# Kernel tuning notes

Hardware: AMD Instinct MI355X
Metric: run time of the kernel (lower is better)

The kernel has to match this reference:

```python
import jax, jax.numpy as jnp
import numpy as np
from jax import lax

TAU = 10.0
THR = 1.0
ALPHA = float(np.exp(-1.0 / TAU))  # leak factor exp(-dt/tau), dt=1


def conv2d(x, w, pad):
    # x: [N,C,H,W], w: [O,I,kh,kw]
    return lax.conv_general_dilated(
        x, w, window_strides=(1, 1), padding=[(pad, pad), (pad, pad)],
        dimension_numbers=('NCHW', 'OIHW', 'NCHW'))


def avgpool(x, k):
    n, c, h, w = x.shape
    return x.reshape(n, c, h // k, k, w // k, k).mean(axis=(3, 5))


def exp_leak(x):
    # x: [T, ...]; v[t] = alpha*v[t-1] + x[t]; outputs membrane each step
    def step(v, xt):
        v = ALPHA * v + xt
        return v, v
    _, y = lax.scan(step, jnp.zeros_like(x[0]), x)
    return y


def lif(x):
    # LIF with SingleSpike + MembraneSubtract reset (norm_input=False)
    def step(v, xt):
        v = ALPHA * v + xt
        s = (v >= THR).astype(v.dtype)
        return v - s * THR, s
    _, s = lax.scan(step, jnp.zeros_like(x[0]), x)
    return s


def forward(x, conv1_w, conv2_w, lin_w):
    B, T = x.shape[:2]
    h = avgpool(conv2d(x.reshape(B * T, 2, 32, 32), conv1_w, 2), 4)  # [BT,4,8,8]
    h = h.reshape(B, T, 4, 8, 8).swapaxes(0, 1)                       # [T,B,4,8,8]
    h = lif(exp_leak(h)).swapaxes(0, 1).reshape(B * T, 4, 8, 8)
    h = avgpool(conv2d(h, conv2_w, 1), 2)                             # [BT,8,4,4]
    h = h.reshape(B, T, 8, 4, 4).swapaxes(0, 1)                       # [T,B,8,4,4]
    h = lif(exp_leak(h)).swapaxes(0, 1).reshape(B, T, 8 * 4 * 4)      # [B,T,128]
    return jnp.einsum('btf,of->bto', h, lin_w)                        # [B,T,2]


def setup_inputs() -> dict:
    key = jax.random.key(0)
    k1, k2, k3, k4 = jax.random.split(key, 4)
    B, T = 128, 100
    x = jax.random.uniform(k1, (B, T, 2, 32, 32), dtype=jnp.float32)
    conv1_w = jax.random.normal(k2, (4, 2, 5, 5), dtype=jnp.float32) / np.sqrt(2 * 5 * 5)
    conv2_w = jax.random.normal(k3, (8, 4, 3, 3), dtype=jnp.float32) / np.sqrt(4 * 3 * 3)
    lin_w = jax.random.normal(k4, (2, 128), dtype=jnp.float32) / np.sqrt(128)
    return {'x': x, 'conv1_w': conv1_w, 'conv2_w': conv2_w, 'lin_w': lin_w}


def reference(x, conv1_w, conv2_w, lin_w):
    return forward(x, conv1_w, conv2_w, lin_w)
```

## Files before the change

kernel.cpp:

```cpp
#include <hip/hip_runtime.h>

#define ALPHA 0.90483741803595957f

__global__ void prep_weights(const float* __restrict__ w1, const float* __restrict__ w2,
                             float* __restrict__ w1e, float* __restrict__ w2e) {
    int idx = blockIdx.x * 256 + threadIdx.x;
    if (idx < 512) {
        int v = idx & 7, u = (idx >> 3) & 7, ch = (idx >> 6) & 1, oc = idx >> 7;
        float s = 0.f;
        for (int a = 0; a < 5; ++a) {
            int i = u - a; if (i < 0 || i > 3) continue;
            for (int b = 0; b < 5; ++b) {
                int j = v - b; if (j < 0 || j > 3) continue;
                s += w1[((oc * 2 + ch) * 5 + a) * 5 + b];
            }
        }
        w1e[idx] = s * (1.f / 16.f);
    } else if (idx < 1024) {
        int k = idx - 512;
        int v = k & 3, u = (k >> 2) & 3, ch = (k >> 4) & 3, oc = k >> 6;
        float s = 0.f;
        for (int a = 0; a < 3; ++a) {
            int i = u - a; if (i < 0 || i > 1) continue;
            for (int b = 0; b < 3; ++b) {
                int j = v - b; if (j < 0 || j > 1) continue;
                s += w2[((oc * 4 + ch) * 3 + a) * 3 + b];
            }
        }
        w2e[k] = s * 0.25f;
    }
}

__global__ __launch_bounds__(256) void conv1_pool(const float* __restrict__ x,
                                                  const float* __restrict__ w1e,
                                                  float* __restrict__ y1) {
    __shared__ __align__(16) float tile[4][2][36][36];
    int tid = threadIdx.x;

    float4* t4 = (float4*)&tile[0][0][0][0];
    #pragma unroll
    for (int k = 0; k < 11; ++k) {
        int i = tid + k * 256;
        if (i < 2592) t4[i] = make_float4(0.f, 0.f, 0.f, 0.f);
    }
    __syncthreads();

    int li = tid >> 6, pos = tid & 63;
    long gi = (long)blockIdx.x * 4 + li;
    const float* src = x + gi * 2048;
    #pragma unroll
    for (int k = 0; k < 8; ++k) {
        int e = k * 256 + pos * 4;
        float4 d = *(const float4*)(src + e);
        int ch = e >> 10, rem = e & 1023, r = rem >> 5, c = rem & 31;
        float* dst = &tile[li][ch][r + 2][c + 2];
        dst[0] = d.x; dst[1] = d.y; dst[2] = d.z; dst[3] = d.w;
    }
    __syncthreads();

    int p = pos >> 3, q = pos & 7;
    float acc0 = 0.f, acc1 = 0.f, acc2 = 0.f, acc3 = 0.f;
    #pragma unroll
    for (int ch = 0; ch < 2; ++ch) {
        #pragma unroll
        for (int r = 0; r < 8; ++r) {
            const float* row = &tile[li][ch][4 * p + r][4 * q];
            float4 a = *(const float4*)row;
            float4 b = *(const float4*)(row + 4);
            float in[8] = {a.x, a.y, a.z, a.w, b.x, b.y, b.z, b.w};
            #pragma unroll
            for (int c = 0; c < 8; ++c) {
                float xi = in[c];
                acc0 += w1e[((0 * 2 + ch) * 8 + r) * 8 + c] * xi;
                acc1 += w1e[((1 * 2 + ch) * 8 + r) * 8 + c] * xi;
                acc2 += w1e[((2 * 2 + ch) * 8 + r) * 8 + c] * xi;
                acc3 += w1e[((3 * 2 + ch) * 8 + r) * 8 + c] * xi;
            }
        }
    }
    float* dst = y1 + gi * 256 + pos;
    dst[0] = acc0; dst[64] = acc1; dst[128] = acc2; dst[192] = acc3;
}

__global__ __launch_bounds__(64, 1) void fused_wave(const float* __restrict__ y1,
                                                    const float* __restrict__ w2e,
                                                    const float* __restrict__ lw,
                                                    float* __restrict__ out) {
    __shared__ float tEv[808];
    __shared__ float tOd[808];
    int lane = threadIdx.x;
    int b = blockIdx.x;

    #pragma unroll
    for (int k = 0; k < 13; ++k) {
        int i = lane + k * 64;
        if (i < 808) { tEv[i] = 0.f; tOd[i] = 0.f; }
    }

    int r1 = lane >> 3, c1 = lane & 7;
    int posq = ((r1 + 1) * 10 + (c1 + 1)) * 4;
    float* wrE0 = &tEv[posq];
    float* wrE1 = &tEv[404 + posq];
    float* wrO0 = &tOd[posq];
    float* wrO1 = &tOd[404 + posq];

    int oc = lane >> 4, p = (lane >> 2) & 3, q = lane & 3;

    float wa[64], wb[64];
    #pragma unroll
    for (int k = 0; k < 16; ++k) {
        float4 ta = *(const float4*)(w2e + oc * 64 + k * 4);
        float4 tb = *(const float4*)(w2e + (oc + 4) * 64 + k * 4);
        wa[k * 4 + 0] = ta.x; wa[k * 4 + 1] = ta.y; wa[k * 4 + 2] = ta.z; wa[k * 4 + 3] = ta.w;
        wb[k * 4 + 0] = tb.x; wb[k * 4 + 1] = tb.y; wb[k * 4 + 2] = tb.z; wb[k * 4 + 3] = tb.w;
    }

    int rbq = ((2 * p) * 10 + 2 * q) * 4 + ((p & 1) ? 404 : 0);
    const float* rbE = &tEv[rbq];
    const float* rbO = &tOd[rbq];

    float lw0a = lw[lane],       lw0b = lw[lane + 64];
    float lw1a = lw[lane + 128], lw1b = lw[lane + 192];

    const float* src = y1 + (long)b * 25600 + lane;
    float* outp = out + (long)b * 200;

    float cur0 = src[0],   cur1 = src[64],  cur2 = src[128], cur3 = src[192];
    float nx0  = src[256], nx1  = src[320], nx2  = src[384], nx3  = src[448];
    float v10 = 0.f, v20 = 0.f, v11 = 0.f, v21 = 0.f;
    float v12 = 0.f, v22 = 0.f, v13 = 0.f, v23 = 0.f;
    float w1a = 0.f, w2a = 0.f, w1b = 0.f, w2b = 0.f;

    for (int tt = 0; tt < 50; ++tt) {
        int tA = 2 * tt;
        const float* nsA = src + (tA + 2 < 100 ? (tA + 2) * 256 : 0);
        float pA0 = nsA[0], pA1 = nsA[64], pA2 = nsA[128], pA3 = nsA[192];

        v10 = ALPHA * v10 + cur0; v20 = ALPHA * v20 + v10;
        float sA0 = (v20 >= 1.f) ? 1.f : 0.f; v20 -= sA0;
        v11 = ALPHA * v11 + cur1; v21 = ALPHA * v21 + v11;
        float sA1 = (v21 >= 1.f) ? 1.f : 0.f; v21 -= sA1;
        v12 = ALPHA * v12 + cur2; v22 = ALPHA * v22 + v12;
        float sA2 = (v22 >= 1.f) ? 1.f : 0.f; v22 -= sA2;
        v13 = ALPHA * v13 + cur3; v23 = ALPHA * v23 + v13;
        float sA3 = (v23 >= 1.f) ? 1.f : 0.f; v23 -= sA3;

        float4 spA = make_float4(sA0, sA1, sA2, sA3);
        *(float4*)wrE0 = spA;
        *(float4*)wrE1 = spA;

        float qa[64];
        #pragma unroll
        for (int rr = 0; rr < 4; ++rr) {
            #pragma unroll
            for (int cc = 0; cc < 4; ++cc) {
                float4 tq = *(const float4*)(rbE + rr * 40 + cc * 4);
                int o = (rr * 4 + cc) * 4;
                qa[o + 0] = tq.x; qa[o + 1] = tq.y; qa[o + 2] = tq.z; qa[o + 3] = tq.w;
            }
        }
        float accaA = 0.f, accbA = 0.f;
        #pragma unroll
        for (int ch = 0; ch < 4; ++ch)
            #pragma unroll
            for (int rr = 0; rr < 4; ++rr)
                #pragma unroll
                for (int cc = 0; cc < 4; ++cc) {
                    float xv = qa[(rr * 4 + cc) * 4 + ch];
                    accaA += wa[ch * 16 + rr * 4 + cc] * xv;
                    accbA += wb[ch * 16 + rr * 4 + cc] * xv;
                }
        w1a = ALPHA * w1a + accaA; w2a = ALPHA * w2a + w1a;
        float saA = (w2a >= 1.f) ? 1.f : 0.f; w2a -= saA;
        w1b = ALPHA * w1b + accbA; w2b = ALPHA * w2b + w1b;
        float sbA = (w2b >= 1.f) ? 1.f : 0.f; w2b -= sbA;

        int tB = tA + 1;
        const float* nsB = src + (tB + 2 < 100 ? (tB + 2) * 256 : 0);
        float pB0 = nsB[0], pB1 = nsB[64], pB2 = nsB[128], pB3 = nsB[192];

        v10 = ALPHA * v10 + nx0; v20 = ALPHA * v20 + v10;
        float sB0 = (v20 >= 1.f) ? 1.f : 0.f; v20 -= sB0;
        v11 = ALPHA * v11 + nx1; v21 = ALPHA * v21 + v11;
        float sB1 = (v21 >= 1.f) ? 1.f : 0.f; v21 -= sB1;
        v12 = ALPHA * v12 + nx2; v22 = ALPHA * v22 + v12;
        float sB2 = (v22 >= 1.f) ? 1.f : 0.f; v22 -= sB2;
        v13 = ALPHA * v13 + nx3; v23 = ALPHA * v23 + v13;
        float sB3 = (v23 >= 1.f) ? 1.f : 0.f; v23 -= sB3;

        float4 spB = make_float4(sB0, sB1, sB2, sB3);
        *(float4*)wrO0 = spB;
        *(float4*)wrO1 = spB;

        float qb[64];
        #pragma unroll
        for (int rr = 0; rr < 4; ++rr) {
            #pragma unroll
            for (int cc = 0; cc < 4; ++cc) {
                float4 tq = *(const float4*)(rbO + rr * 40 + cc * 4);
                int o = (rr * 4 + cc) * 4;
                qb[o + 0] = tq.x; qb[o + 1] = tq.y; qb[o + 2] = tq.z; qb[o + 3] = tq.w;
            }
        }
        float accaB = 0.f, accbB = 0.f;
        #pragma unroll
        for (int ch = 0; ch < 4; ++ch)
            #pragma unroll
            for (int rr = 0; rr < 4; ++rr)
                #pragma unroll
                for (int cc = 0; cc < 4; ++cc) {
                    float xv = qb[(rr * 4 + cc) * 4 + ch];
                    accaB += wa[ch * 16 + rr * 4 + cc] * xv;
                    accbB += wb[ch * 16 + rr * 4 + cc] * xv;
                }
        w1a = ALPHA * w1a + accaB; w2a = ALPHA * w2a + w1a;
        float saB = (w2a >= 1.f) ? 1.f : 0.f; w2a -= saB;
        w1b = ALPHA * w1b + accbB; w2b = ALPHA * w2b + w1b;
        float sbB = (w2b >= 1.f) ? 1.f : 0.f; w2b -= sbB;

        float a0 = saA * lw0a + sbA * lw0b;
        float a1 = saA * lw1a + sbA * lw1b;
        float b0 = saB * lw0a + sbB * lw0b;
        float b1 = saB * lw1a + sbB * lw1b;
        #pragma unroll
        for (int off = 32; off; off >>= 1) {
            a0 += __shfl_xor(a0, off);
            a1 += __shfl_xor(a1, off);
            b0 += __shfl_xor(b0, off);
            b1 += __shfl_xor(b1, off);
        }
        if (lane == 0) {
            *(float2*)(outp + tA * 2) = make_float2(a0, a1);
            *(float2*)(outp + tB * 2) = make_float2(b0, b1);
        }

        cur0 = pA0; cur1 = pA1; cur2 = pA2; cur3 = pA3;
        nx0 = pB0; nx1 = pB1; nx2 = pB2; nx3 = pB3;
    }
}

extern "C" void kernel_launch(void* const* d_in, const int* in_sizes, int n_in,
                              void* d_out, int out_size, void* d_ws, size_t ws_size,
                              hipStream_t stream) {
    const float* x  = (const float*)d_in[0];
    const float* w1 = (const float*)d_in[1];
    const float* w2 = (const float*)d_in[2];
    const float* lw = (const float*)d_in[3];
    float* out = (float*)d_out;

    float* ws   = (float*)d_ws;
    float* w1e  = ws;
    float* w2e  = ws + 512;
    float* y1   = ws + 1024;

    prep_weights<<<4, 256, 0, stream>>>(w1, w2, w1e, w2e);
    conv1_pool<<<3200, 256, 0, stream>>>(x, w1e, y1);
    fused_wave<<<128, 64, 0, stream>>>(y1, w2e, lw, out);
}
```

Measured before the change: 212.2 us.

## Software-pipeline layer-1 LIF one step ahead of layer-2 conv in fused wave kernel

Restructures the per-batch time loop so the layer-1 spike computation for step t+1 runs while the layer-2 convolution reads step t's spikes from shared memory, using a prologue and epilogue. The global-load prefetch distance is also raised from two to four timesteps. The aim is to break the serial dependency chain inside each step and hide LDS and global load latency in a single-wave block. The cost is more live registers, which risks spills given the 128 weight registers already held, and more code.

```diff
diff --git a/kernel.cpp b/kernel.cpp
--- a/kernel.cpp
+++ b/kernel.cpp
@@ -86,23 +86,23 @@
                                                     const float* __restrict__ w2e,
                                                     const float* __restrict__ lw,
                                                     float* __restrict__ out) {
-    __shared__ float tEv[808];
-    __shared__ float tOd[808];
+    __shared__ float tE[808];
+    __shared__ float tO[808];
     int lane = threadIdx.x;
     int b = blockIdx.x;
 
     #pragma unroll
     for (int k = 0; k < 13; ++k) {
         int i = lane + k * 64;
-        if (i < 808) { tEv[i] = 0.f; tOd[i] = 0.f; }
+        if (i < 808) { tE[i] = 0.f; tO[i] = 0.f; }
     }
 
     int r1 = lane >> 3, c1 = lane & 7;
     int posq = ((r1 + 1) * 10 + (c1 + 1)) * 4;
-    float* wrE0 = &tEv[posq];
-    float* wrE1 = &tEv[404 + posq];
-    float* wrO0 = &tOd[posq];
-    float* wrO1 = &tOd[404 + posq];
+    float* wE0 = &tE[posq];
+    float* wE1 = &tE[404 + posq];
+    float* wO0 = &tO[posq];
+    float* wO1 = &tO[404 + posq];
 
     int oc = lane >> 4, p = (lane >> 2) & 3, q = lane & 3;
 
@@ -116,8 +116,8 @@
     }
 
     int rbq = ((2 * p) * 10 + 2 * q) * 4 + ((p & 1) ? 404 : 0);
-    const float* rbE = &tEv[rbq];
-    const float* rbO = &tOd[rbq];
+    const float* rbE = &tE[rbq];
+    const float* rbO = &tO[rbq];
 
     float lw0a = lw[lane],       lw0b = lw[lane + 64];
     float lw1a = lw[lane + 128], lw1b = lw[lane + 192];
@@ -125,29 +125,36 @@
     const float* src = y1 + (long)b * 25600 + lane;
     float* outp = out + (long)b * 200;
 
-    float cur0 = src[0],   cur1 = src[64],  cur2 = src[128], cur3 = src[192];
-    float nx0  = src[256], nx1  = src[320], nx2  = src[384], nx3  = src[448];
+    float x0  = src[0],    x1  = src[64],   x2  = src[128],  x3  = src[192];
+    float c10 = src[256],  c11 = src[320],  c12 = src[384],  c13 = src[448];
+    float c20 = src[512],  c21 = src[576],  c22 = src[640],  c23 = src[704];
+    float p10 = src[768],  p11 = src[832],  p12 = src[896],  p13 = src[960];
+    float p20 = src[1024], p21 = src[1088], p22 = src[1152], p23 = src[1216];
+
     float v10 = 0.f, v20 = 0.f, v11 = 0.f, v21 = 0.f;
     float v12 = 0.f, v22 = 0.f, v13 = 0.f, v23 = 0.f;
     float w1a = 0.f, w2a = 0.f, w1b = 0.f, w2b = 0.f;
 
-    for (int tt = 0; tt < 50; ++tt) {
-        int tA = 2 * tt;
-        const float* nsA = src + (tA + 2 < 100 ? (tA + 2) * 256 : 0);
-        float pA0 = nsA[0], pA1 = nsA[64], pA2 = nsA[128], pA3 = nsA[192];
-
-        v10 = ALPHA * v10 + cur0; v20 = ALPHA * v20 + v10;
-        float sA0 = (v20 >= 1.f) ? 1.f : 0.f; v20 -= sA0;
-        v11 = ALPHA * v11 + cur1; v21 = ALPHA * v21 + v11;
-        float sA1 = (v21 >= 1.f) ? 1.f : 0.f; v21 -= sA1;
-        v12 = ALPHA * v12 + cur2; v22 = ALPHA * v22 + v12;
-        float sA2 = (v22 >= 1.f) ? 1.f : 0.f; v22 -= sA2;
-        v13 = ALPHA * v13 + cur3; v23 = ALPHA * v23 + v13;
-        float sA3 = (v23 >= 1.f) ? 1.f : 0.f; v23 -= sA3;
-
-        float4 spA = make_float4(sA0, sA1, sA2, sA3);
-        *(float4*)wrE0 = spA;
-        *(float4*)wrE1 = spA;
+    {
+        v10 = ALPHA * v10 + x0; v20 = ALPHA * v20 + v10;
+        float s0 = (v20 >= 1.f) ? 1.f : 0.f; v20 -= s0;
+        v11 = ALPHA * v11 + x1; v21 = ALPHA * v21 + v11;
+        float s1 = (v21 >= 1.f) ? 1.f : 0.f; v21 -= s1;
+        v12 = ALPHA * v12 + x2; v22 = ALPHA * v22 + v12;
+        float s2 = (v22 >= 1.f) ? 1.f : 0.f; v22 -= s2;
+        v13 = ALPHA * v13 + x3; v23 = ALPHA * v23 + v13;
+        float s3 = (v23 >= 1.f) ? 1.f : 0.f; v23 -= s3;
+        float4 sp = make_float4(s0, s1, s2, s3);
+        *(float4*)wE0 = sp;
+        *(float4*)wE1 = sp;
+    }
+
+    for (int i = 0; i < 49; ++i) {
+        int t5 = 2 * i + 5, t6 = 2 * i + 6;
+        const float* a5 = src + (t5 < 100 ? t5 * 256 : 0);
+        const float* a6 = src + (t6 < 100 ? t6 * 256 : 0);
+        float n10 = a5[0], n11 = a5[64], n12 = a5[128], n13 = a5[192];
+        float n20 = a6[0], n21 = a6[64], n22 = a6[128], n23 = a6[192];
 
         float qa[64];
         #pragma unroll
@@ -159,7 +166,20 @@
                 qa[o + 0] = tq.x; qa[o + 1] = tq.y; qa[o + 2] = tq.z; qa[o + 3] = tq.w;
             }
         }
-        float accaA = 0.f, accbA = 0.f;
+
+        v10 = ALPHA * v10 + c10; v20 = ALPHA * v20 + v10;
+        float sA0 = (v20 >= 1.f) ? 1.f : 0.f; v20 -= sA0;
+        v11 = ALPHA * v11 + c11; v21 = ALPHA * v21 + v11;
+        float sA1 = (v21 >= 1.f) ? 1.f : 0.f; v21 -= sA1;
+        v12 = ALPHA * v12 + c12; v22 = ALPHA * v22 + v12;
+        float sA2 = (v22 >= 1.f) ? 1.f : 0.f; v22 -= sA2;
+        v13 = ALPHA * v13 + c13; v23 = ALPHA * v23 + v13;
+        float sA3 = (v23 >= 1.f) ? 1.f : 0.f; v23 -= sA3;
+        float4 spA = make_float4(sA0, sA1, sA2, sA3);
+        *(float4*)wO0 = spA;
+        *(float4*)wO1 = spA;
+
+        float accaE = 0.f, accbE = 0.f;
         #pragma unroll
         for (int ch = 0; ch < 4; ++ch)
             #pragma unroll
@@ -167,30 +187,13 @@
                 #pragma unroll
                 for (int cc = 0; cc < 4; ++cc) {
                     float xv = qa[(rr * 4 + cc) * 4 + ch];
-                    accaA += wa[ch * 16 + rr * 4 + cc] * xv;
-                    accbA += wb[ch * 16 + rr * 4 + cc] * xv;
+                    accaE += wa[ch * 16 + rr * 4 + cc] * xv;
+                    accbE += wb[ch * 16 + rr * 4 + cc] * xv;
                 }
-        w1a = ALPHA * w1a + accaA; w2a = ALPHA * w2a + w1a;
-        float saA = (w2a >= 1.f) ? 1.f : 0.f; w2a -= saA;
-        w1b = ALPHA * w1b + accbA; w2b = ALPHA * w2b + w1b;
-        float sbA = (w2b >= 1.f) ? 1.f : 0.f; w2b -= sbA;
-
-        int tB = tA + 1;
-        const float* nsB = src + (tB + 2 < 100 ? (tB + 2) * 256 : 0);
-        float pB0 = nsB[0], pB1 = nsB[64], pB2 = nsB[128], pB3 = nsB[192];
-
-        v10 = ALPHA * v10 + nx0; v20 = ALPHA * v20 + v10;
-        float sB0 = (v20 >= 1.f) ? 1.f : 0.f; v20 -= sB0;
-        v11 = ALPHA * v11 + nx1; v21 = ALPHA * v21 + v11;
-        float sB1 = (v21 >= 1.f) ? 1.f : 0.f; v21 -= sB1;
-        v12 = ALPHA * v12 + nx2; v22 = ALPHA * v22 + v12;
-        float sB2 = (v22 >= 1.f) ? 1.f : 0.f; v22 -= sB2;
-        v13 = ALPHA * v13 + nx3; v23 = ALPHA * v23 + v13;
-        float sB3 = (v23 >= 1.f) ? 1.f : 0.f; v23 -= sB3;
-
-        float4 spB = make_float4(sB0, sB1, sB2, sB3);
-        *(float4*)wrO0 = spB;
-        *(float4*)wrO1 = spB;
+        w1a = ALPHA * w1a + accaE; w2a = ALPHA * w2a + w1a;
+        float saE = (w2a >= 1.f) ? 1.f : 0.f; w2a -= saE;
+        w1b = ALPHA * w1b + accbE; w2b = ALPHA * w2b + w1b;
+        float sbE = (w2b >= 1.f) ? 1.f : 0.f; w2b -= sbE;
 
         float qb[64];
         #pragma unroll
@@ -202,7 +205,20 @@
                 qb[o + 0] = tq.x; qb[o + 1] = tq.y; qb[o + 2] = tq.z; qb[o + 3] = tq.w;
             }
         }
-        float accaB = 0.f, accbB = 0.f;
+
+        v10 = ALPHA * v10 + c20; v20 = ALPHA * v20 + v10;
+        float sB0 = (v20 >= 1.f) ? 1.f : 0.f; v20 -= sB0;
+        v11 = ALPHA * v11 + c21; v21 = ALPHA * v21 + v11;
+        float sB1 = (v21 >= 1.f) ? 1.f : 0.f; v21 -= sB1;
+        v12 = ALPHA * v12 + c22; v22 = ALPHA * v22 + v12;
+        float sB2 = (v22 >= 1.f) ? 1.f : 0.f; v22 -= sB2;
+        v13 = ALPHA * v13 + c23; v23 = ALPHA * v23 + v13;
+        float sB3 = (v23 >= 1.f) ? 1.f : 0.f; v23 -= sB3;
+        float4 spB = make_float4(sB0, sB1, sB2, sB3);
+        *(float4*)wE0 = spB;
+        *(float4*)wE1 = spB;
+
+        float accaO = 0.f, accbO = 0.f;
         #pragma unroll
         for (int ch = 0; ch < 4; ++ch)
             #pragma unroll
@@ -210,18 +226,18 @@
                 #pragma unroll
                 for (int cc = 0; cc < 4; ++cc) {
                     float xv = qb[(rr * 4 + cc) * 4 + ch];
-                    accaB += wa[ch * 16 + rr * 4 + cc] * xv;
-                    accbB += wb[ch * 16 + rr * 4 + cc] * xv;
+                    accaO += wa[ch * 16 + rr * 4 + cc] * xv;
+                    accbO += wb[ch * 16 + rr * 4 + cc] * xv;
                 }
-        w1a = ALPHA * w1a + accaB; w2a = ALPHA * w2a + w1a;
-        float saB = (w2a >= 1.f) ? 1.f : 0.f; w2a -= saB;
-        w1b = ALPHA * w1b + accbB; w2b = ALPHA * w2b + w1b;
-        float sbB = (w2b >= 1.f) ? 1.f : 0.f; w2b -= sbB;
-
-        float a0 = saA * lw0a + sbA * lw0b;
-        float a1 = saA * lw1a + sbA * lw1b;
-        float b0 = saB * lw0a + sbB * lw0b;
-        float b1 = saB * lw1a + sbB * lw1b;
+        w1a = ALPHA * w1a + accaO; w2a = ALPHA * w2a + w1a;
+        float saO = (w2a >= 1.f) ? 1.f : 0.f; w2a -= saO;
+        w1b = ALPHA * w1b + accbO; w2b = ALPHA * w2b + w1b;
+        float sbO = (w2b >= 1.f) ? 1.f : 0.f; w2b -= sbO;
+
+        float a0 = saE * lw0a + sbE * lw0b;
+        float a1 = saE * lw1a + sbE * lw1b;
+        float b0 = saO * lw0a + sbO * lw0b;
+        float b1 = saO * lw1a + sbO * lw1b;
         #pragma unroll
         for (int off = 32; off; off >>= 1) {
             a0 += __shfl_xor(a0, off);
@@ -230,12 +246,97 @@
             b1 += __shfl_xor(b1, off);
         }
         if (lane == 0) {
-            *(float2*)(outp + tA * 2) = make_float2(a0, a1);
-            *(float2*)(outp + tB * 2) = make_float2(b0, b1);
-        }
-
-        cur0 = pA0; cur1 = pA1; cur2 = pA2; cur3 = pA3;
-        nx0 = pB0; nx1 = pB1; nx2 = pB2; nx3 = pB3;
+            *(float2*)(outp + 4 * i)     = make_float2(a0, a1);
+            *(float2*)(outp + 4 * i + 2) = make_float2(b0, b1);
+        }
+
+        c10 = p10; c11 = p11; c12 = p12; c13 = p13;
+        c20 = p20; c21 = p21; c22 = p22; c23 = p23;
+        p10 = n10; p11 = n11; p12 = n12; p13 = n13;
+        p20 = n20; p21 = n21; p22 = n22; p23 = n23;
+    }
+
+    {
+        float qa[64];
+        #pragma unroll
+        for (int rr = 0; rr < 4; ++rr) {
+            #pragma unroll
+            for (int cc = 0; cc < 4; ++cc) {
+                float4 tq = *(const float4*)(rbE + rr * 40 + cc * 4);
+                int o = (rr * 4 + cc) * 4;
+                qa[o + 0] = tq.x; qa[o + 1] = tq.y; qa[o + 2] = tq.z; qa[o + 3] = tq.w;
+            }
+        }
+
+        v10 = ALPHA * v10 + c10; v20 = ALPHA * v20 + v10;
+        float sA0 = (v20 >= 1.f) ? 1.f : 0.f; v20 -= sA0;
+        v11 = ALPHA * v11 + c11; v21 = ALPHA * v21 + v11;
+        float sA1 = (v21 >= 1.f) ? 1.f : 0.f; v21 -= sA1;
+        v12 = ALPHA * v12 + c12; v22 = ALPHA * v22 + v12;
+        float sA2 = (v22 >= 1.f) ? 1.f : 0.f; v22 -= sA2;
+        v13 = ALPHA * v13 + c13; v23 = ALPHA * v23 + v13;
+        float sA3 = (v23 >= 1.f) ? 1.f : 0.f; v23 -= sA3;
+        float4 spA = make_float4(sA0, sA1, sA2, sA3);
+        *(float4*)wO0 = spA;
+        *(float4*)wO1 = spA;
+
+        float accaE = 0.f, accbE = 0.f;
+        #pragma unroll
+        for (int ch = 0; ch < 4; ++ch)
+            #pragma unroll
+            for (int rr = 0; rr < 4; ++rr)
+                #pragma unroll
+                for (int cc = 0; cc < 4; ++cc) {
+                    float xv = qa[(rr * 4 + cc) * 4 + ch];
+                    accaE += wa[ch * 16 + rr * 4 + cc] * xv;
+                    accbE += wb[ch * 16 + rr * 4 + cc] * xv;
+                }
+        w1a = ALPHA * w1a + accaE; w2a = ALPHA * w2a + w1a;
+        float saE = (w2a >= 1.f) ? 1.f : 0.f; w2a -= saE;
+        w1b = ALPHA * w1b + accbE; w2b = ALPHA * w2b + w1b;
+        float sbE = (w2b >= 1.f) ? 1.f : 0.f; w2b -= sbE;
+
+        float qb[64];
+        #pragma unroll
+        for (int rr = 0; rr < 4; ++rr) {
+            #pragma unroll
+            for (int cc = 0; cc < 4; ++cc) {
+                float4 tq = *(const float4*)(rbO + rr * 40 + cc * 4);
+                int o = (rr * 4 + cc) * 4;
+                qb[o + 0] = tq.x; qb[o + 1] = tq.y; qb[o + 2] = tq.z; qb[o + 3] = tq.w;
+            }
+        }
+        float accaO = 0.f, accbO = 0.f;
+        #pragma unroll
+        for (int ch = 0; ch < 4; ++ch)
+            #pragma unroll
+            for (int rr = 0; rr < 4; ++rr)
+                #pragma unroll
+                for (int cc = 0; cc < 4; ++cc) {
+                    float xv = qb[(rr * 4 + cc) * 4 + ch];
+                    accaO += wa[ch * 16 + rr * 4 + cc] * xv;
+                    accbO += wb[ch * 16 + rr * 4 + cc] * xv;
+                }
+        w1a = ALPHA * w1a + accaO; w2a = ALPHA * w2a + w1a;
+        float saO = (w2a >= 1.f) ? 1.f : 0.f; w2a -= saO;
+        w1b = ALPHA * w1b + accbO; w2b = ALPHA * w2b + w1b;
+        float sbO = (w2b >= 1.f) ? 1.f : 0.f; w2b -= sbO;
+
+        float a0 = saE * lw0a + sbE * lw0b;
+        float a1 = saE * lw1a + sbE * lw1b;
+        float b0 = saO * lw0a + sbO * lw0b;
+        float b1 = saO * lw1a + sbO * lw1b;
+        #pragma unroll
+        for (int off = 32; off; off >>= 1) {
+            a0 += __shfl_xor(a0, off);
+            a1 += __shfl_xor(a1, off);
+            b0 += __shfl_xor(b0, off);
+            b1 += __shfl_xor(b1, off);
+        }
+        if (lane == 0) {
+            *(float2*)(outp + 196) = make_float2(a0, a1);
+            *(float2*)(outp + 198) = make_float2(b0, b1);
+        }
     }
 }
 
```

Measured after the change: 211.6 us. Within noise of the previous version (-0.3%).
